# Kernel optimization log

Measured on AMD Instinct MI355X. Metric: run time of the kernel, lower is better.

## Reference

```python
import jax, jax.numpy as jnp
import numpy as np


def setup_inputs() -> dict:
    key = jax.random.key(0)
    k_x, k0, k1, k2, kb = jax.random.split(key, 5)
    D, C, KH, KW = 256, 128, 3, 3
    R1, R2 = 8, 4
    x = jax.random.normal(k_x, (32, C, 64, 64), dtype=jnp.float32)
    # TT cores (leading/trailing rank-1 dims squeezed), init U(-0.77, 0.77) as in the torch module
    core0 = jax.random.uniform(k0, (D, C, R1), dtype=jnp.float32, minval=-0.77, maxval=0.77)
    core1 = jax.random.uniform(k1, (D, R1, KH, R2), dtype=jnp.float32, minval=-0.77, maxval=0.77)
    core2 = jax.random.uniform(k2, (D, R2, KW), dtype=jnp.float32, minval=-0.77, maxval=0.77)
    bias = jax.random.uniform(kb, (1,), dtype=jnp.float32, minval=-0.1, maxval=0.1)
    return {"x": x, "core0": core0, "core1": core1, "core2": core2,
            "bias": bias, "stride": 1, "pad": 1}


def reference(x, core0, core1, core2, bias, stride, pad):
    # Reconstruct the full conv kernel from the TT cores: [D, C, kH, kW]
    kernel = jnp.einsum('dcr,drks,dsj->dckj', core0, core1, core2)
    # Same math as pad + unfold + einsum('nchwkj,dckj->ndhw'): a standard cross-correlation conv
    out = jax.lax.conv_general_dilated(
        x, kernel,
        window_strides=(stride, stride),
        padding=[(pad, pad), (pad, pad)],
        dimension_numbers=('NCHW', 'OIHW', 'NCHW'))
    # scalar bias broadcast over all output channels (bias.view(1,-1,1,1) with 1 element)
    return out + bias.reshape(1, -1, 1, 1)
```

## Files before the change

### kernel.cpp

```cpp
#include <hip/hip_runtime.h>

typedef __bf16 bf16x8 __attribute__((ext_vector_type(8)));
typedef float f32x4 __attribute__((ext_vector_type(4)));

__device__ __forceinline__ unsigned short f2bf(float f) {
    union { float f; unsigned int u; } v; v.f = f;
    unsigned int u = v.u;
    unsigned int r = (u + 0x7fffu + ((u >> 16) & 1u)) >> 16;
    return (unsigned short)r;
}

__global__ void build_w_kernel(const float* __restrict__ core0,
                               const float* __restrict__ core1,
                               const float* __restrict__ core2,
                               unsigned short* __restrict__ wb) {
    __shared__ float s1[96];
    __shared__ float s2[12];
    const int d = blockIdx.x;
    const int c = threadIdx.x;
    if (c < 96) s1[c] = core1[d * 96 + c];
    if (c >= 96 && c < 108) s2[c - 96] = core2[d * 12 + (c - 96)];
    __syncthreads();
    float t0[8];
#pragma unroll
    for (int r = 0; r < 8; ++r) t0[r] = core0[(d * 128 + c) * 8 + r];
#pragma unroll
    for (int kh = 0; kh < 3; ++kh) {
        float v[4] = {0.f, 0.f, 0.f, 0.f};
#pragma unroll
        for (int r = 0; r < 8; ++r)
#pragma unroll
            for (int s = 0; s < 4; ++s)
                v[s] += t0[r] * s1[(r * 3 + kh) * 4 + s];
#pragma unroll
        for (int kw = 0; kw < 3; ++kw) {
            float val = 0.f;
#pragma unroll
            for (int s = 0; s < 4; ++s) val += v[s] * s2[s * 3 + kw];
            const int kidx = (kh * 3 + kw) * 128 + c;
            wb[(kidx >> 3) * 2048 + d * 8 + (kidx & 7)] = f2bf(val);
        }
    }
}

#define LC 136

__global__ __launch_bounds__(256, 3) void conv_mfma_kernel(
    const float* __restrict__ x, const unsigned short* __restrict__ wb,
    const float* __restrict__ bias, float* __restrict__ out) {
    __shared__ __align__(16) unsigned short xl[3 * 66 * LC];

    const int tid  = threadIdx.x;
    const int lane = tid & 63;
    const int wv   = tid >> 6;
    const int l15  = lane & 15;
    const int quad = lane >> 4;
    const int bid  = blockIdx.x;
    const int n    = bid >> 6;
    const int h    = bid & 63;

    if (tid < 96) {
        const int row = tid >> 5;
        const int j   = tid & 31;
        const int col = (j >> 4) ? 65 : 0;
        const int c   = (j & 15) << 3;
        *(uint4*)(xl + (row * 66 + col) * LC + c) = make_uint4(0u, 0u, 0u, 0u);
    }

#pragma unroll 2
    for (int i = 0; i < 6; ++i) {
        const int it  = tid + (i << 8);
        const int w4  = it & 15;
        const int cg  = (it >> 4) & 31;
        const int row = it >> 9;
        const int rimg = h + row - 1;
        float4 p0 = make_float4(0.f, 0.f, 0.f, 0.f), p1 = p0, p2 = p0, p3 = p0;
        const int c = cg << 2;
        const int w = w4 << 2;
        if (rimg >= 0 && rimg < 64) {
            const float4* gp = (const float4*)(x + (((n * 128 + c) * 64 + rimg) * 64 + w));
            p0 = gp[0];
            p1 = gp[1024];
            p2 = gp[2048];
            p3 = gp[3072];
        }
        unsigned short* base = xl + (row * 66 + w + 1) * LC + c;
        *(ushort4*)(base)          = make_ushort4(f2bf(p0.x), f2bf(p1.x), f2bf(p2.x), f2bf(p3.x));
        *(ushort4*)(base + LC)     = make_ushort4(f2bf(p0.y), f2bf(p1.y), f2bf(p2.y), f2bf(p3.y));
        *(ushort4*)(base + 2 * LC) = make_ushort4(f2bf(p0.z), f2bf(p1.z), f2bf(p2.z), f2bf(p3.z));
        *(ushort4*)(base + 3 * LC) = make_ushort4(f2bf(p0.w), f2bf(p1.w), f2bf(p2.w), f2bf(p3.w));
    }
    __syncthreads();

    f32x4 acc[4][4];
#pragma unroll
    for (int a0 = 0; a0 < 4; ++a0)
#pragma unroll
        for (int b0 = 0; b0 < 4; ++b0) acc[a0][b0] = (f32x4){0.f, 0.f, 0.f, 0.f};

    const int dwave = wv << 6;
    const bf16x8* wgv = (const bf16x8*)wb;
    const int abase = quad * 256 + dwave + l15;

    bf16x8 an[4];
#pragma unroll
    for (int dt = 0; dt < 4; ++dt) an[dt] = wgv[abase + dt * 16];

    const unsigned short* bb = xl + l15 * LC + quad * 8;

#pragma unroll
    for (int tap = 0; tap < 9; ++tap) {
        const int kh = tap / 3;
        const int kw = tap - kh * 3;
#pragma unroll
        for (int c4 = 0; c4 < 4; ++c4) {
            const int ch = tap * 4 + c4;
            bf16x8 ac[4];
#pragma unroll
            for (int dt = 0; dt < 4; ++dt) ac[dt] = an[dt];
            if (ch + 1 < 36) {
                const bf16x8* g2 = wgv + (ch + 1) * 1024 + abase;
#pragma unroll
                for (int dt = 0; dt < 4; ++dt) an[dt] = g2[dt * 16];
            }
            const int c0 = c4 << 5;
            bf16x8 bfr[4];
            const unsigned short* bp = bb + (kh * 66 + kw) * LC + c0;
#pragma unroll
            for (int pt = 0; pt < 4; ++pt) bfr[pt] = *(const bf16x8*)(bp + pt * 16 * LC);
#pragma unroll
            for (int dt = 0; dt < 4; ++dt)
#pragma unroll
                for (int pt = 0; pt < 4; ++pt)
                    acc[dt][pt] = __builtin_amdgcn_mfma_f32_16x16x32_bf16(
                        ac[dt], bfr[pt], acc[dt][pt], 0, 0, 0);
        }
    }

    const float bv = bias[0];
#pragma unroll
    for (int dt = 0; dt < 4; ++dt) {
#pragma unroll
        for (int pt = 0; pt < 4; ++pt) {
#pragma unroll
            for (int r = 0; r < 4; ++r) {
                const int d = dwave + dt * 16 + quad * 4 + r;
                const int w = pt * 16 + l15;
                out[((n * 256 + d) * 64 + h) * 64 + w] = acc[dt][pt][r] + bv;
            }
        }
    }
}

extern "C" void kernel_launch(void* const* d_in, const int* in_sizes, int n_in,
                              void* d_out, int out_size, void* d_ws, size_t ws_size,
                              hipStream_t stream) {
    const float* x     = (const float*)d_in[0];
    const float* core0 = (const float*)d_in[1];
    const float* core1 = (const float*)d_in[2];
    const float* core2 = (const float*)d_in[3];
    const float* bias  = (const float*)d_in[4];
    unsigned short* wb = (unsigned short*)d_ws;

    build_w_kernel<<<256, 128, 0, stream>>>(core0, core1, core2, wb);
    conv_mfma_kernel<<<2048, 256, 0, stream>>>(x, wb, bias, (float*)d_out);
}
```

Before: 240.0 us.

## Process four output rows per block with rolling three-row LDS buffer and prefetch

Each block now computes four consecutive output rows instead of one, keeping a circular three-row bf16 input buffer in LDS so every input row is loaded and converted once per block rather than three times. The next input row is loaded from global into registers while the current row's MFMAs run, then written to LDS between barriers. The grid shrinks from 2048 to 512 blocks and the occupancy hint drops to two blocks per SM, which increases register room but reduces parallelism and adds two barriers per row.

```diff
diff --git a/kernel.cpp b/kernel.cpp
--- a/kernel.cpp
+++ b/kernel.cpp
@@ -45,7 +45,7 @@
 
 #define LC 136
 
-__global__ __launch_bounds__(256, 3) void conv_mfma_kernel(
+__global__ __launch_bounds__(256, 2) void conv_mfma_kernel(
     const float* __restrict__ x, const unsigned short* __restrict__ wb,
     const float* __restrict__ bias, float* __restrict__ out) {
     __shared__ __align__(16) unsigned short xl[3 * 66 * LC];
@@ -56,99 +56,124 @@
     const int l15  = lane & 15;
     const int quad = lane >> 4;
     const int bid  = blockIdx.x;
-    const int n    = bid >> 6;
-    const int h    = bid & 63;
+    const int n    = bid >> 4;
+    const int h0   = (bid & 15) << 2;
+
+    const int sw4  = tid & 15;
+    const int scg0 = tid >> 4;
 
     if (tid < 96) {
-        const int row = tid >> 5;
+        const int s   = tid >> 5;
         const int j   = tid & 31;
         const int col = (j >> 4) ? 65 : 0;
         const int c   = (j & 15) << 3;
-        *(uint4*)(xl + (row * 66 + col) * LC + c) = make_uint4(0u, 0u, 0u, 0u);
+        *(uint4*)(xl + (s * 66 + col) * LC + c) = make_uint4(0u, 0u, 0u, 0u);
     }
 
-#pragma unroll 2
-    for (int i = 0; i < 6; ++i) {
-        const int it  = tid + (i << 8);
-        const int w4  = it & 15;
-        const int cg  = (it >> 4) & 31;
-        const int row = it >> 9;
-        const int rimg = h + row - 1;
-        float4 p0 = make_float4(0.f, 0.f, 0.f, 0.f), p1 = p0, p2 = p0, p3 = p0;
-        const int c = cg << 2;
-        const int w = w4 << 2;
-        if (rimg >= 0 && rimg < 64) {
-            const float4* gp = (const float4*)(x + (((n * 128 + c) * 64 + rimg) * 64 + w));
-            p0 = gp[0];
-            p1 = gp[1024];
-            p2 = gp[2048];
-            p3 = gp[3072];
+    float4 st[2][4];
+
+    auto stage_load = [&](int rimg) {
+#pragma unroll
+        for (int i = 0; i < 2; ++i) {
+            const float4 z = make_float4(0.f, 0.f, 0.f, 0.f);
+            st[i][0] = z; st[i][1] = z; st[i][2] = z; st[i][3] = z;
+            if (rimg >= 0 && rimg < 64) {
+                const int c = (scg0 + (i << 4)) << 2;
+                const float4* gp = (const float4*)(x + (((n * 128 + c) * 64 + rimg) * 64) + (sw4 << 2));
+                st[i][0] = gp[0];
+                st[i][1] = gp[1024];
+                st[i][2] = gp[2048];
+                st[i][3] = gp[3072];
+            }
         }
-        unsigned short* base = xl + (row * 66 + w + 1) * LC + c;
-        *(ushort4*)(base)          = make_ushort4(f2bf(p0.x), f2bf(p1.x), f2bf(p2.x), f2bf(p3.x));
-        *(ushort4*)(base + LC)     = make_ushort4(f2bf(p0.y), f2bf(p1.y), f2bf(p2.y), f2bf(p3.y));
-        *(ushort4*)(base + 2 * LC) = make_ushort4(f2bf(p0.z), f2bf(p1.z), f2bf(p2.z), f2bf(p3.z));
-        *(ushort4*)(base + 3 * LC) = make_ushort4(f2bf(p0.w), f2bf(p1.w), f2bf(p2.w), f2bf(p3.w));
+    };
+
+    auto stage_write = [&](int slot) {
+#pragma unroll
+        for (int i = 0; i < 2; ++i) {
+            const int c = (scg0 + (i << 4)) << 2;
+            unsigned short* base = xl + (slot * 66 + (sw4 << 2) + 1) * LC + c;
+            *(ushort4*)(base)          = make_ushort4(f2bf(st[i][0].x), f2bf(st[i][1].x), f2bf(st[i][2].x), f2bf(st[i][3].x));
+            *(ushort4*)(base + LC)     = make_ushort4(f2bf(st[i][0].y), f2bf(st[i][1].y), f2bf(st[i][2].y), f2bf(st[i][3].y));
+            *(ushort4*)(base + 2 * LC) = make_ushort4(f2bf(st[i][0].z), f2bf(st[i][1].z), f2bf(st[i][2].z), f2bf(st[i][3].z));
+            *(ushort4*)(base + 3 * LC) = make_ushort4(f2bf(st[i][0].w), f2bf(st[i][1].w), f2bf(st[i][2].w), f2bf(st[i][3].w));
+        }
+    };
+
+#pragma unroll 1
+    for (int k = 0; k < 3; ++k) {
+        const int rimg = h0 - 1 + k;
+        stage_load(rimg);
+        stage_write((rimg + 3) % 3);
     }
     __syncthreads();
-
-    f32x4 acc[4][4];
-#pragma unroll
-    for (int a0 = 0; a0 < 4; ++a0)
-#pragma unroll
-        for (int b0 = 0; b0 < 4; ++b0) acc[a0][b0] = (f32x4){0.f, 0.f, 0.f, 0.f};
 
     const int dwave = wv << 6;
     const bf16x8* wgv = (const bf16x8*)wb;
     const int abase = quad * 256 + dwave + l15;
+    const unsigned short* bb = xl + l15 * LC + quad * 8;
+    const float bv = bias[0];
 
     bf16x8 an[4];
 #pragma unroll
     for (int dt = 0; dt < 4; ++dt) an[dt] = wgv[abase + dt * 16];
 
-    const unsigned short* bb = xl + l15 * LC + quad * 8;
+#pragma unroll 1
+    for (int r = 0; r < 4; ++r) {
+        const int oh = h0 + r;
+
+        if (r < 3) stage_load(oh + 2);
+
+        f32x4 acc[4][4];
+#pragma unroll
+        for (int a0 = 0; a0 < 4; ++a0)
+#pragma unroll
+            for (int b0 = 0; b0 < 4; ++b0) acc[a0][b0] = (f32x4){0.f, 0.f, 0.f, 0.f};
 
 #pragma unroll
-    for (int tap = 0; tap < 9; ++tap) {
-        const int kh = tap / 3;
-        const int kw = tap - kh * 3;
+        for (int tap = 0; tap < 9; ++tap) {
+            const int kh = tap / 3;
+            const int kw = tap - kh * 3;
+            const int slot = (oh + 2 + kh) % 3;
+            const unsigned short* bt = bb + (slot * 66 + kw) * LC;
 #pragma unroll
-        for (int c4 = 0; c4 < 4; ++c4) {
-            const int ch = tap * 4 + c4;
-            bf16x8 ac[4];
+            for (int c4 = 0; c4 < 4; ++c4) {
+                const int ch = tap * 4 + c4;
+                bf16x8 ac[4];
 #pragma unroll
-            for (int dt = 0; dt < 4; ++dt) ac[dt] = an[dt];
-            if (ch + 1 < 36) {
-                const bf16x8* g2 = wgv + (ch + 1) * 1024 + abase;
+                for (int dt = 0; dt < 4; ++dt) ac[dt] = an[dt];
+                const int nc = (ch + 1 == 36) ? 0 : ch + 1;
+                const bf16x8* g2 = wgv + nc * 1024 + abase;
 #pragma unroll
                 for (int dt = 0; dt < 4; ++dt) an[dt] = g2[dt * 16];
-            }
-            const int c0 = c4 << 5;
-            bf16x8 bfr[4];
-            const unsigned short* bp = bb + (kh * 66 + kw) * LC + c0;
+                const int c0 = c4 << 5;
+                bf16x8 bfr[4];
+                const unsigned short* bp = bt + c0;
 #pragma unroll
-            for (int pt = 0; pt < 4; ++pt) bfr[pt] = *(const bf16x8*)(bp + pt * 16 * LC);
+                for (int pt = 0; pt < 4; ++pt) bfr[pt] = *(const bf16x8*)(bp + pt * 16 * LC);
 #pragma unroll
-            for (int dt = 0; dt < 4; ++dt)
+                for (int dt = 0; dt < 4; ++dt)
 #pragma unroll
-                for (int pt = 0; pt < 4; ++pt)
-                    acc[dt][pt] = __builtin_amdgcn_mfma_f32_16x16x32_bf16(
-                        ac[dt], bfr[pt], acc[dt][pt], 0, 0, 0);
-        }
-    }
-
-    const float bv = bias[0];
-#pragma unroll
-    for (int dt = 0; dt < 4; ++dt) {
-#pragma unroll
-        for (int pt = 0; pt < 4; ++pt) {
-#pragma unroll
-            for (int r = 0; r < 4; ++r) {
-                const int d = dwave + dt * 16 + quad * 4 + r;
-                const int w = pt * 16 + l15;
-                out[((n * 256 + d) * 64 + h) * 64 + w] = acc[dt][pt][r] + bv;
+                    for (int pt = 0; pt < 4; ++pt)
+                        acc[dt][pt] = __builtin_amdgcn_mfma_f32_16x16x32_bf16(
+                            ac[dt], bfr[pt], acc[dt][pt], 0, 0, 0);
             }
         }
+
+        __syncthreads();
+        if (r < 3) stage_write((oh + 2) % 3);
+        __syncthreads();
+
+#pragma unroll
+        for (int dt = 0; dt < 4; ++dt)
+#pragma unroll
+            for (int pt = 0; pt < 4; ++pt)
+#pragma unroll
+                for (int rr = 0; rr < 4; ++rr) {
+                    const int d = dwave + dt * 16 + quad * 4 + rr;
+                    const int w = pt * 16 + l15;
+                    out[((n * 256 + d) * 64 + oh) * 64 + w] = acc[dt][pt][rr] + bv;
+                }
     }
 }
 
@@ -163,5 +188,5 @@
     unsigned short* wb = (unsigned short*)d_ws;
 
     build_w_kernel<<<256, 128, 0, stream>>>(core0, core1, core2, wb);
-    conv_mfma_kernel<<<2048, 256, 0, stream>>>(x, wb, bias, (float*)d_out);
+    conv_mfma_kernel<<<512, 256, 0, stream>>>(x, wb, bias, (float*)d_out);
 }
```

After: 462.4 us. 92.7% more time.

## Compute two output rows per block to reuse weights and halo rows

Applied to the files above, without the earlier changes.

Each block now produces two adjacent output rows instead of one. It stages four input rows in LDS instead of three and keeps two accumulator sets, so every weight fragment loaded from global memory feeds twice as many MFMAs. This halves global weight traffic per output and cuts the redundant halo-row loads from 3x to 2x. In exchange it doubles accumulator registers, lowers the occupancy hint from 3 to 2 blocks, enlarges LDS per block, and halves the grid to 1024 blocks.

```diff
diff --git a/kernel.cpp b/kernel.cpp
--- a/kernel.cpp
+++ b/kernel.cpp
@@ -45,10 +45,10 @@
 
 #define LC 136
 
-__global__ __launch_bounds__(256, 3) void conv_mfma_kernel(
+__global__ __launch_bounds__(256, 2) void conv_mfma_kernel(
     const float* __restrict__ x, const unsigned short* __restrict__ wb,
     const float* __restrict__ bias, float* __restrict__ out) {
-    __shared__ __align__(16) unsigned short xl[3 * 66 * LC];
+    __shared__ __align__(16) unsigned short xl[4 * 66 * LC];
 
     const int tid  = threadIdx.x;
     const int lane = tid & 63;
@@ -56,24 +56,24 @@
     const int l15  = lane & 15;
     const int quad = lane >> 4;
     const int bid  = blockIdx.x;
-    const int n    = bid >> 6;
-    const int h    = bid & 63;
+    const int n    = bid >> 5;
+    const int h0   = (bid & 31) << 1;
 
-    if (tid < 96) {
-        const int row = tid >> 5;
+    if (tid < 128) {
+        const int s   = tid >> 5;
         const int j   = tid & 31;
         const int col = (j >> 4) ? 65 : 0;
         const int c   = (j & 15) << 3;
-        *(uint4*)(xl + (row * 66 + col) * LC + c) = make_uint4(0u, 0u, 0u, 0u);
+        *(uint4*)(xl + (s * 66 + col) * LC + c) = make_uint4(0u, 0u, 0u, 0u);
     }
 
 #pragma unroll 2
-    for (int i = 0; i < 6; ++i) {
+    for (int i = 0; i < 8; ++i) {
         const int it  = tid + (i << 8);
         const int w4  = it & 15;
         const int cg  = (it >> 4) & 31;
         const int row = it >> 9;
-        const int rimg = h + row - 1;
+        const int rimg = h0 + row - 1;
         float4 p0 = make_float4(0.f, 0.f, 0.f, 0.f), p1 = p0, p2 = p0, p3 = p0;
         const int c = cg << 2;
         const int w = w4 << 2;
@@ -92,11 +92,14 @@
     }
     __syncthreads();
 
-    f32x4 acc[4][4];
+    f32x4 acc0[4][4], acc1[4][4];
 #pragma unroll
     for (int a0 = 0; a0 < 4; ++a0)
 #pragma unroll
-        for (int b0 = 0; b0 < 4; ++b0) acc[a0][b0] = (f32x4){0.f, 0.f, 0.f, 0.f};
+        for (int b0 = 0; b0 < 4; ++b0) {
+            acc0[a0][b0] = (f32x4){0.f, 0.f, 0.f, 0.f};
+            acc1[a0][b0] = (f32x4){0.f, 0.f, 0.f, 0.f};
+        }
 
     const int dwave = wv << 6;
     const bf16x8* wgv = (const bf16x8*)wb;
@@ -124,16 +127,22 @@
                 for (int dt = 0; dt < 4; ++dt) an[dt] = g2[dt * 16];
             }
             const int c0 = c4 << 5;
-            bf16x8 bfr[4];
-            const unsigned short* bp = bb + (kh * 66 + kw) * LC + c0;
+            bf16x8 bfr0[4], bfr1[4];
+            const unsigned short* bp0 = bb + (kh * 66 + kw) * LC + c0;
 #pragma unroll
-            for (int pt = 0; pt < 4; ++pt) bfr[pt] = *(const bf16x8*)(bp + pt * 16 * LC);
+            for (int pt = 0; pt < 4; ++pt) {
+                bfr0[pt] = *(const bf16x8*)(bp0 + pt * 16 * LC);
+                bfr1[pt] = *(const bf16x8*)(bp0 + 66 * LC + pt * 16 * LC);
+            }
 #pragma unroll
             for (int dt = 0; dt < 4; ++dt)
 #pragma unroll
-                for (int pt = 0; pt < 4; ++pt)
-                    acc[dt][pt] = __builtin_amdgcn_mfma_f32_16x16x32_bf16(
-                        ac[dt], bfr[pt], acc[dt][pt], 0, 0, 0);
+                for (int pt = 0; pt < 4; ++pt) {
+                    acc0[dt][pt] = __builtin_amdgcn_mfma_f32_16x16x32_bf16(
+                        ac[dt], bfr0[pt], acc0[dt][pt], 0, 0, 0);
+                    acc1[dt][pt] = __builtin_amdgcn_mfma_f32_16x16x32_bf16(
+                        ac[dt], bfr1[pt], acc1[dt][pt], 0, 0, 0);
+                }
         }
     }
 
@@ -143,10 +152,11 @@
 #pragma unroll
         for (int pt = 0; pt < 4; ++pt) {
 #pragma unroll
-            for (int r = 0; r < 4; ++r) {
-                const int d = dwave + dt * 16 + quad * 4 + r;
+            for (int rr = 0; rr < 4; ++rr) {
+                const int d = dwave + dt * 16 + quad * 4 + rr;
                 const int w = pt * 16 + l15;
-                out[((n * 256 + d) * 64 + h) * 64 + w] = acc[dt][pt][r] + bv;
+                out[((n * 256 + d) * 64 + h0) * 64 + w]     = acc0[dt][pt][rr] + bv;
+                out[((n * 256 + d) * 64 + h0 + 1) * 64 + w] = acc1[dt][pt][rr] + bv;
             }
         }
     }
@@ -163,5 +173,5 @@
     unsigned short* wb = (unsigned short*)d_ws;
 
     build_w_kernel<<<256, 128, 0, stream>>>(core0, core1, core2, wb);
-    conv_mfma_kernel<<<2048, 256, 0, stream>>>(x, wb, bias, (float*)d_out);
+    conv_mfma_kernel<<<1024, 256, 0, stream>>>(x, wb, bias, (float*)d_out);
 }
```

New measurement: 382.2 us. +59.3%, slower.
